# Optimization experiments

Measured on AMD Instinct MI355X. Metric: run time of the kernel, lower is better.

The kernel has to match this reference:

```python
import jax, jax.numpy as jnp
import numpy as np

# ---- static configuration (mirrors C4WithSyscalls __init__/_build_keys) ----
MEM = 16384            # memory_size
OUT = 64               # output_size
NCTX = MEM + 5 + OUT   # context: [memory, PC, SP, BP, AX, OUT_LEN, output]
SCALE = 10.0
GATE_SCALE = 20.0
ADDR_BITS = int(np.ceil(np.log2(NCTX)))   # 15
TYPE_BITS = 5
KDIM = ADDR_BITS + TYPE_BITS
POWERS = jnp.asarray(2 ** np.arange(ADDR_BITS), jnp.int32)

# opcode values for the 15 experts: IMM,LEA,ADD,SUB,MUL,DIV,MOD,SHL,SHR,EQ,NE,LT,GT,LE,GE
OP_VALS = jnp.asarray([1., 2., 9., 10., 11., 12., 13., 14., 15., 3., 4., 5., 6., 7., 8.], jnp.float32)
# binary ops (everything except IMM, LEA) pop the stack: sp += 8
POP_MASK = jnp.asarray([0., 0.] + [1.] * 13, jnp.float32)


def _build_keys():
    addrs = np.arange(NCTX)
    bits = (addrs[:, None] // (2 ** np.arange(ADDR_BITS))) % 2
    addr_keys = (2.0 * bits - 1.0) * SCALE                       # [N, ADDR_BITS]
    type_tags = np.full((NCTX, TYPE_BITS), -SCALE)
    type_tags[MEM, 0] = SCALE      # PC
    type_tags[MEM + 1, 1] = SCALE  # SP
    type_tags[MEM + 2, 2] = SCALE  # BP
    type_tags[MEM + 3, 3] = SCALE  # AX
    type_tags[MEM + 4:, 4] = SCALE  # OUT_LEN + output slots
    return jnp.asarray(np.concatenate([addr_keys, type_tags], 1), jnp.float32)

KEYS = _build_keys()  # [NCTX, KDIM]


def silu_threshold(x, scale=GATE_SCALE):
    d = scale * x
    return (jax.nn.silu(d + 0.5 * scale) - jax.nn.silu(d - 0.5 * scale)) / scale


def eq_gate(a, b, scale=GATE_SCALE):
    diff = a - b
    return silu_threshold(diff + 0.5, scale) * silu_threshold(-diff + 0.5, scale)


def attend(context, addr):
    """Soft-addressed gather: context [B,NCTX], addr [B] float -> (value [B], weights [B,NCTX])."""
    ai = jnp.clip(addr, 0.0, float(NCTX - 1)).astype(jnp.int32)
    bits = (ai[:, None] // POWERS) % 2
    addr_q = (2.0 * bits.astype(jnp.float32) - 1.0) * SCALE                 # [B, ADDR_BITS]
    type_q = jnp.full((addr.shape[0], TYPE_BITS), -SCALE, jnp.float32)      # memory_type tag
    q = jnp.concatenate([addr_q, type_q], axis=1)                           # [B, KDIM]
    scores = jnp.einsum('nd,bd->bn', KEYS, q) / np.sqrt(KDIM)
    w = jax.nn.softmax(scores, axis=1)
    return jnp.einsum('bn,bn->b', w, context), w


def expert_outputs(a, b, imm, bp):
    """a = stack_top, b = ax. Returns [B, 15] new-ax candidates per expert."""
    safeb = jnp.where(jnp.abs(b) < 1e-6, 1e-6, b)
    div = a / safeb
    mod = a - safeb * jnp.floor(div)
    sh = jnp.clip(b, 0.0, 31.0)
    eq = eq_gate(a, b)
    lt = jax.nn.sigmoid(GATE_SCALE * (b - a - 0.5))
    gt = jax.nn.sigmoid(GATE_SCALE * (a - b - 0.5))
    return jnp.stack([
        imm,               # IMM
        bp + imm,          # LEA
        a + b,             # ADD
        a - b,             # SUB
        a * b,             # MUL
        div,               # DIV
        mod,               # MOD
        a * jnp.exp2(sh),  # SHL
        a * jnp.exp2(-sh), # SHR
        eq,                # EQ
        1.0 - eq,          # NE
        lt,                # LT
        gt,                # GT
        1.0 - gt,          # LE
        1.0 - lt,          # GE
    ], axis=-1)


def _forward(memory, output, ax, pc, sp, bp, out_len, num_steps):
    B = memory.shape[0]
    pcf, spf, bpf = pc.astype(jnp.float32), sp.astype(jnp.float32), bp.astype(jnp.float32)
    olf = out_len.astype(jnp.float32)[:, None]

    def step(carry, _):
        pc_, sp_, bp_, ax_, mem_ = carry
        regs = jnp.stack([pc_, sp_, bp_, ax_], axis=1)                    # [B,4]
        context = jnp.concatenate([mem_, regs, olf, output], axis=1)     # [B,NCTX]
        inst, _ = attend(context, pc_)
        imm = jnp.floor(inst / 256.0)
        opcode = inst - imm * 256.0
        stack_top, w_sp = attend(context, sp_)
        gates = eq_gate(opcode[:, None], OP_VALS[None, :])                # [B,15] soft top-1
        outs = expert_outputs(stack_top, ax_, imm, bp_)                   # [B,15]
        gsum = gates.sum(-1)
        new_ax = (gates * outs).sum(-1) + (1.0 - gsum) * ax_              # NoOp default
        pop_g = (gates * POP_MASK).sum(-1)
        new_sp = sp_ + 8.0 * pop_g
        new_pc = pc_ + 8.0
        # soft scatter: write new_ax back at the (soft) stack-top address
        new_mem = mem_ + pop_g[:, None] * w_sp[:, :MEM] * (new_ax[:, None] - mem_)
        return (new_pc, new_sp, bp_, new_ax, new_mem), None

    carry, _ = jax.lax.scan(step, (pcf, spf, bpf, ax, memory), None, length=num_steps)
    return carry[4]  # final memory [B, MEM]


def setup_inputs() -> dict:
    key = jax.random.key(0)
    k = jax.random.split(key, 8)
    B = 1024
    return {
        'memory': jax.random.normal(k[0], (B, MEM), jnp.float32),
        'output': jax.random.normal(k[1], (B, OUT), jnp.float32),
        'ax': jax.random.normal(k[2], (B,), jnp.float32),
        'pc': jax.random.randint(k[3], (B,), 0, MEM, jnp.int32),
        'sp': jax.random.randint(k[4], (B,), 0, MEM, jnp.int32),
        'bp': jax.random.randint(k[5], (B,), 0, MEM, jnp.int32),
        'out_len': jax.random.randint(k[6], (B,), 0, OUT, jnp.int32),
        'num_steps': 16,
    }


def reference(memory, output, ax, pc, sp, bp, out_len, num_steps):
    return _forward(memory, output, ax, pc, sp, bp, out_len, num_steps)
```

## Files before the change

kernel.cpp:

```cpp
#include <hip/hip_runtime.h>
#include <math.h>

#define MEMSZ 16384
#define NCTX  16453

__device__ __forceinline__ float sigmoidf_(float x) {
    return 1.0f / (1.0f + __expf(-x));
}
__device__ __forceinline__ float siluf_(float x) {
    return x * sigmoidf_(x);
}
__device__ __forceinline__ float silu_thr(float x) {
    float d = 20.0f * x;
    return (siluf_(d + 10.0f) - siluf_(d - 10.0f)) * 0.05f;
}
__device__ __forceinline__ float eq_gate_d(float diff) {
    return silu_thr(diff + 0.5f) * silu_thr(0.5f - diff);
}

__global__ void copy_kernel(const float4* __restrict__ src,
                            float4* __restrict__ dst, int n4) {
    int i = blockIdx.x * blockDim.x + threadIdx.x;
    if (i < n4) dst[i] = src[i];
}

__global__ void sim_kernel(float* __restrict__ mem,
                           const float* __restrict__ outp,
                           const float* __restrict__ ax_in,
                           const int* __restrict__ pc_in,
                           const int* __restrict__ sp_in,
                           const int* __restrict__ bp_in,
                           const int* __restrict__ ol_in,
                           const int* __restrict__ nstep,
                           int B) {
    int b = blockIdx.x * blockDim.x + threadIdx.x;
    if (b >= B) return;

    float* __restrict__ mrow = mem + (size_t)b * MEMSZ;
    const float* __restrict__ orow = outp + (size_t)b * 64;

    float pc  = (float)pc_in[b];
    float sp  = (float)sp_in[b];
    float bp  = (float)bp_in[b];
    float ax  = ax_in[b];
    float olf = (float)ol_in[b];
    int   T   = nstep[0];

    const float opv[15] = {1.f, 2.f, 9.f, 10.f, 11.f, 12.f, 13.f, 14.f, 15.f,
                           3.f, 4.f, 5.f, 6.f, 7.f, 8.f};

    for (int t = 0; t < T; ++t) {
        float a1 = fminf(fmaxf(pc, 0.0f), (float)(NCTX - 1));
        int ai = (int)a1;
        float inst;
        if (ai < MEMSZ) {
            inst = mrow[ai];
        } else {
            int r = ai - MEMSZ;
            float cv = (r == 0) ? pc
                     : (r == 1) ? sp
                     : (r == 2) ? bp
                     : (r == 3) ? ax
                     : (r == 4) ? olf
                                : orow[r - 5];
            inst = 0.5f * (cv + mrow[ai - MEMSZ]);
        }
        float imm = floorf(inst * (1.0f / 256.0f));
        float opc = inst - imm * 256.0f;

        float a2 = fminf(fmaxf(sp, 0.0f), (float)(NCTX - 1));
        int si = (int)a2;
        int target = (si < MEMSZ) ? si : (si - MEMSZ);
        float mtv = mrow[target];
        float stv, wfac;
        if (si < MEMSZ) {
            stv = mtv;
            wfac = 1.0f;
        } else {
            int r = si - MEMSZ;
            float cv = (r == 0) ? pc
                     : (r == 1) ? sp
                     : (r == 2) ? bp
                     : (r == 3) ? ax
                     : (r == 4) ? olf
                                : orow[r - 5];
            stv = 0.5f * (cv + mtv);
            wfac = 0.5f;
        }

        float a = stv, bv = ax;
        float safeb = (fabsf(bv) < 1e-6f) ? 1e-6f : bv;
        float dv = a / safeb;
        float md = a - safeb * floorf(dv);
        float sh = fminf(fmaxf(bv, 0.0f), 31.0f);
        float eq = eq_gate_d(a - bv);
        float lt = sigmoidf_(20.0f * (bv - a - 0.5f));
        float gt = sigmoidf_(20.0f * (a - bv - 0.5f));
        float outs[15] = {
            imm,
            bp + imm,
            a + bv,
            a - bv,
            a * bv,
            dv,
            md,
            a * exp2f(sh),
            a * exp2f(-sh),
            eq,
            1.0f - eq,
            lt,
            gt,
            1.0f - gt,
            1.0f - lt
        };

        float gsum = 0.0f, acc = 0.0f, pop = 0.0f;
#pragma unroll
        for (int j = 0; j < 15; ++j) {
            float g = eq_gate_d(opc - opv[j]);
            gsum += g;
            acc += g * outs[j];
            if (j >= 2) pop += g;
        }
        float nax = acc + (1.0f - gsum) * ax;

        mrow[target] = mtv + pop * wfac * (nax - mtv);

        sp = sp + 8.0f * pop;
        pc = pc + 8.0f;
        ax = nax;
    }
}

extern "C" void kernel_launch(void* const* d_in, const int* in_sizes, int n_in,
                              void* d_out, int out_size, void* d_ws, size_t ws_size,
                              hipStream_t stream) {
    const float* memory = (const float*)d_in[0];
    const float* output = (const float*)d_in[1];
    const float* ax     = (const float*)d_in[2];
    const int*   pc     = (const int*)d_in[3];
    const int*   sp     = (const int*)d_in[4];
    const int*   bp     = (const int*)d_in[5];
    const int*   ol     = (const int*)d_in[6];
    const int*   ns     = (const int*)d_in[7];

    int B = in_sizes[0] / MEMSZ;
    int n = B * MEMSZ;
    int n4 = n / 4;

    float* out = (float*)d_out;

    hipLaunchKernelGGL(copy_kernel, dim3((n4 + 255) / 256), dim3(256), 0, stream,
                       (const float4*)memory, (float4*)out, n4);
    hipLaunchKernelGGL(sim_kernel, dim3((B + 255) / 256), dim3(256), 0, stream,
                       out, output, ax, pc, sp, bp, ol, ns, B);
}
```

Baseline: 170.7 us.

## Fuse copy and simulation into one block-per-row kernel staged through LDS

Replaces the separate copy kernel and the thread-per-row simulation kernel with one kernel that gives each batch row its own block. The block loads the 64KB memory row into shared memory with nontemporal loads, runs the serial step loop on thread 0 against LDS, then writes the row out with nontemporal stores. This removes the second kernel launch and the scattered, latency-bound global reads and writes of the old simulation kernel. In exchange, 64KB of LDS per block limits occupancy, and the serial section leaves 255 threads idle between the barriers.

```diff
diff --git a/kernel.cpp b/kernel.cpp
--- a/kernel.cpp
+++ b/kernel.cpp
@@ -3,6 +3,8 @@
 
 #define MEMSZ 16384
 #define NCTX  16453
+
+typedef float f4 __attribute__((ext_vector_type(4)));
 
 __device__ __forceinline__ float sigmoidf_(float x) {
     return 1.0f / (1.0f + __expf(-x));
@@ -18,117 +20,135 @@
     return silu_thr(diff + 0.5f) * silu_thr(0.5f - diff);
 }
 
-__global__ void copy_kernel(const float4* __restrict__ src,
-                            float4* __restrict__ dst, int n4) {
-    int i = blockIdx.x * blockDim.x + threadIdx.x;
-    if (i < n4) dst[i] = src[i];
-}
+__global__ __launch_bounds__(256) void fused_sim_kernel(
+        const float* __restrict__ memory,
+        const float* __restrict__ outp,
+        const float* __restrict__ ax_in,
+        const int*   __restrict__ pc_in,
+        const int*   __restrict__ sp_in,
+        const int*   __restrict__ bp_in,
+        const int*   __restrict__ ol_in,
+        const int*   __restrict__ nstep,
+        float*       __restrict__ dst)
+{
+    __shared__ float smem[MEMSZ];
 
-__global__ void sim_kernel(float* __restrict__ mem,
-                           const float* __restrict__ outp,
-                           const float* __restrict__ ax_in,
-                           const int* __restrict__ pc_in,
-                           const int* __restrict__ sp_in,
-                           const int* __restrict__ bp_in,
-                           const int* __restrict__ ol_in,
-                           const int* __restrict__ nstep,
-                           int B) {
-    int b = blockIdx.x * blockDim.x + threadIdx.x;
-    if (b >= B) return;
+    const int b   = blockIdx.x;
+    const int tid = threadIdx.x;
 
-    float* __restrict__ mrow = mem + (size_t)b * MEMSZ;
-    const float* __restrict__ orow = outp + (size_t)b * 64;
+    const f4* __restrict__ src4 = (const f4*)(memory + (size_t)b * MEMSZ);
+    f4*       __restrict__ dst4 = (f4*)(dst + (size_t)b * MEMSZ);
+    f4*       sm4               = (f4*)smem;
 
-    float pc  = (float)pc_in[b];
-    float sp  = (float)sp_in[b];
-    float bp  = (float)bp_in[b];
-    float ax  = ax_in[b];
-    float olf = (float)ol_in[b];
-    int   T   = nstep[0];
+#pragma unroll
+    for (int i = 0; i < 16; ++i) {
+        sm4[tid + i * 256] = __builtin_nontemporal_load(&src4[tid + i * 256]);
+    }
+    __syncthreads();
 
-    const float opv[15] = {1.f, 2.f, 9.f, 10.f, 11.f, 12.f, 13.f, 14.f, 15.f,
-                           3.f, 4.f, 5.f, 6.f, 7.f, 8.f};
+    if (tid == 0) {
+        const float* __restrict__ orow = outp + (size_t)b * 64;
 
-    for (int t = 0; t < T; ++t) {
-        float a1 = fminf(fmaxf(pc, 0.0f), (float)(NCTX - 1));
-        int ai = (int)a1;
-        float inst;
-        if (ai < MEMSZ) {
-            inst = mrow[ai];
-        } else {
-            int r = ai - MEMSZ;
-            float cv = (r == 0) ? pc
-                     : (r == 1) ? sp
-                     : (r == 2) ? bp
-                     : (r == 3) ? ax
-                     : (r == 4) ? olf
-                                : orow[r - 5];
-            inst = 0.5f * (cv + mrow[ai - MEMSZ]);
+        float pc  = (float)pc_in[b];
+        float sp  = (float)sp_in[b];
+        float bp  = (float)bp_in[b];
+        float ax  = ax_in[b];
+        float olf = (float)ol_in[b];
+        int   T   = nstep[0];
+
+        const float opv[15] = {1.f, 2.f, 9.f, 10.f, 11.f, 12.f, 13.f, 14.f, 15.f,
+                               3.f, 4.f, 5.f, 6.f, 7.f, 8.f};
+
+        for (int t = 0; t < T; ++t) {
+            float a1 = fminf(fmaxf(pc, 0.0f), (float)(NCTX - 1));
+            int   ai = (int)a1;
+            float a2 = fminf(fmaxf(sp, 0.0f), (float)(NCTX - 1));
+            int   si = (int)a2;
+            int pidx   = (ai < MEMSZ) ? ai : (ai - MEMSZ);
+            int target = (si < MEMSZ) ? si : (si - MEMSZ);
+            float m_pc = smem[pidx];
+            float mtv  = smem[target];
+
+            float inst;
+            if (ai < MEMSZ) {
+                inst = m_pc;
+            } else {
+                int r = ai - MEMSZ;
+                float cv = (r == 0) ? pc
+                         : (r == 1) ? sp
+                         : (r == 2) ? bp
+                         : (r == 3) ? ax
+                         : (r == 4) ? olf
+                                    : orow[r - 5];
+                inst = 0.5f * (cv + m_pc);
+            }
+            float imm = floorf(inst * (1.0f / 256.0f));
+            float opc = inst - imm * 256.0f;
+
+            float stv, wfac;
+            if (si < MEMSZ) {
+                stv = mtv;
+                wfac = 1.0f;
+            } else {
+                int r = si - MEMSZ;
+                float cv = (r == 0) ? pc
+                         : (r == 1) ? sp
+                         : (r == 2) ? bp
+                         : (r == 3) ? ax
+                         : (r == 4) ? olf
+                                    : orow[r - 5];
+                stv = 0.5f * (cv + mtv);
+                wfac = 0.5f;
+            }
+
+            float a = stv, bv = ax;
+            float safeb = (fabsf(bv) < 1e-6f) ? 1e-6f : bv;
+            float dvv = a / safeb;
+            float md  = a - safeb * floorf(dvv);
+            float sh  = fminf(fmaxf(bv, 0.0f), 31.0f);
+            float eq  = eq_gate_d(a - bv);
+            float lt  = sigmoidf_(20.0f * (bv - a - 0.5f));
+            float gt  = sigmoidf_(20.0f * (a - bv - 0.5f));
+            float outs[15] = {
+                imm,
+                bp + imm,
+                a + bv,
+                a - bv,
+                a * bv,
+                dvv,
+                md,
+                a * exp2f(sh),
+                a * exp2f(-sh),
+                eq,
+                1.0f - eq,
+                lt,
+                gt,
+                1.0f - gt,
+                1.0f - lt
+            };
+
+            float gsum = 0.0f, acc = 0.0f, pop = 0.0f;
+#pragma unroll
+            for (int j = 0; j < 15; ++j) {
+                float g = eq_gate_d(opc - opv[j]);
+                gsum += g;
+                acc  += g * outs[j];
+                if (j >= 2) pop += g;
+            }
+            float nax = acc + (1.0f - gsum) * ax;
+
+            smem[target] = mtv + pop * wfac * (nax - mtv);
+
+            sp = sp + 8.0f * pop;
+            pc = pc + 8.0f;
+            ax = nax;
         }
-        float imm = floorf(inst * (1.0f / 256.0f));
-        float opc = inst - imm * 256.0f;
+    }
+    __syncthreads();
 
-        float a2 = fminf(fmaxf(sp, 0.0f), (float)(NCTX - 1));
-        int si = (int)a2;
-        int target = (si < MEMSZ) ? si : (si - MEMSZ);
-        float mtv = mrow[target];
-        float stv, wfac;
-        if (si < MEMSZ) {
-            stv = mtv;
-            wfac = 1.0f;
-        } else {
-            int r = si - MEMSZ;
-            float cv = (r == 0) ? pc
-                     : (r == 1) ? sp
-                     : (r == 2) ? bp
-                     : (r == 3) ? ax
-                     : (r == 4) ? olf
-                                : orow[r - 5];
-            stv = 0.5f * (cv + mtv);
-            wfac = 0.5f;
-        }
-
-        float a = stv, bv = ax;
-        float safeb = (fabsf(bv) < 1e-6f) ? 1e-6f : bv;
-        float dv = a / safeb;
-        float md = a - safeb * floorf(dv);
-        float sh = fminf(fmaxf(bv, 0.0f), 31.0f);
-        float eq = eq_gate_d(a - bv);
-        float lt = sigmoidf_(20.0f * (bv - a - 0.5f));
-        float gt = sigmoidf_(20.0f * (a - bv - 0.5f));
-        float outs[15] = {
-            imm,
-            bp + imm,
-            a + bv,
-            a - bv,
-            a * bv,
-            dv,
-            md,
-            a * exp2f(sh),
-            a * exp2f(-sh),
-            eq,
-            1.0f - eq,
-            lt,
-            gt,
-            1.0f - gt,
-            1.0f - lt
-        };
-
-        float gsum = 0.0f, acc = 0.0f, pop = 0.0f;
 #pragma unroll
-        for (int j = 0; j < 15; ++j) {
-            float g = eq_gate_d(opc - opv[j]);
-            gsum += g;
-            acc += g * outs[j];
-            if (j >= 2) pop += g;
-        }
-        float nax = acc + (1.0f - gsum) * ax;
-
-        mrow[target] = mtv + pop * wfac * (nax - mtv);
-
-        sp = sp + 8.0f * pop;
-        pc = pc + 8.0f;
-        ax = nax;
+    for (int i = 0; i < 16; ++i) {
+        __builtin_nontemporal_store(sm4[tid + i * 256], &dst4[tid + i * 256]);
     }
 }
 
@@ -145,13 +165,7 @@
     const int*   ns     = (const int*)d_in[7];
 
     int B = in_sizes[0] / MEMSZ;
-    int n = B * MEMSZ;
-    int n4 = n / 4;
 
-    float* out = (float*)d_out;
-
-    hipLaunchKernelGGL(copy_kernel, dim3((n4 + 255) / 256), dim3(256), 0, stream,
-                       (const float4*)memory, (float4*)out, n4);
-    hipLaunchKernelGGL(sim_kernel, dim3((B + 255) / 256), dim3(256), 0, stream,
-                       out, output, ax, pc, sp, bp, ol, ns, B);
+    hipLaunchKernelGGL(fused_sim_kernel, dim3(B), dim3(256), 0, stream,
+                       memory, output, ax, pc, sp, bp, ol, ns, (float*)d_out);
 }
```

Measured after the change: 270.7 us. 58.6% more time.
